# Performance work log

Measured on AMD Instinct MI355X. Metric: run time of the kernel, lower is better.

## Reference

```python
import jax, jax.numpy as jnp
import numpy as np

N = 50000       # nodes
E = 800000      # edges (before self-loops)
G = 64          # graphs in batch
F_IN = 128      # node_features
HID = 64        # hidden_channels
H1 = 8          # conv1 heads
NEG_SLOPE = 0.2
EPS = 1e-16


def _gat_layer(x, src, dst, W, att_src, att_dst, bias, heads, out_ch, concat):
    """PyG GATConv (eval mode: dropout inactive). src/dst include self-loops.
    x: [N, F_in]; W: [F_in, heads*out_ch]; att_*: [heads, out_ch]; bias: [heads*out_ch] or [out_ch]."""
    n = x.shape[0]
    h = (x @ W).reshape(n, heads, out_ch)                 # [N,H,C]
    a_s = jnp.sum(h * att_src, axis=-1)                   # [N,H]
    a_d = jnp.sum(h * att_dst, axis=-1)                   # [N,H]
    e = jax.nn.leaky_relu(a_s[src] + a_d[dst], NEG_SLOPE)  # [Etot,H]
    # segment softmax over incoming edges of each destination node
    m = jax.ops.segment_max(e, dst, num_segments=n)       # [N,H]
    e = jnp.exp(e - m[dst])
    denom = jax.ops.segment_sum(e, dst, num_segments=n)   # [N,H]
    alpha = e / (denom[dst] + EPS)                        # [Etot,H]
    msg = h[src] * alpha[:, :, None]                      # [Etot,H,C]
    out = jax.ops.segment_sum(msg, dst, num_segments=n)   # [N,H,C]
    if concat:
        out = out.reshape(n, heads * out_ch)
    else:
        out = out.mean(axis=1)
    return out + bias


def setup_inputs() -> dict:
    key = jax.random.key(0)
    ks = jax.random.split(key, 14)
    x = jax.random.normal(ks[0], (N, F_IN), dtype=jnp.float32)
    edge_index = jax.random.randint(ks[1], (2, E), 0, N, dtype=jnp.int64)
    batch_index = jnp.sort(jax.random.randint(ks[2], (N,), 0, G, dtype=jnp.int64))
    s = 0.05
    return {
        "x": x,
        "edge_index": edge_index,
        "batch_index": batch_index,
        "W1": jax.random.normal(ks[3], (F_IN, H1 * HID), dtype=jnp.float32) * s,
        "att_src1": jax.random.normal(ks[4], (H1, HID), dtype=jnp.float32) * s,
        "att_dst1": jax.random.normal(ks[5], (H1, HID), dtype=jnp.float32) * s,
        "b1": jnp.zeros((H1 * HID,), dtype=jnp.float32),
        "W2": jax.random.normal(ks[6], (H1 * HID, HID), dtype=jnp.float32) * s,
        "att_src2": jax.random.normal(ks[7], (1, HID), dtype=jnp.float32) * s,
        "att_dst2": jax.random.normal(ks[8], (1, HID), dtype=jnp.float32) * s,
        "b2": jnp.zeros((HID,), dtype=jnp.float32),
        "lin_W": jax.random.normal(ks[9], (HID, 1), dtype=jnp.float32) * s,
        "lin_b": jnp.zeros((1,), dtype=jnp.float32),
    }


def reference(x, edge_index, batch_index, W1, att_src1, att_dst1, b1,
              W2, att_src2, att_dst2, b2, lin_W, lin_b):
    n = x.shape[0]
    loops = jnp.arange(n, dtype=edge_index.dtype)
    src = jnp.concatenate([edge_index[0], loops])
    dst = jnp.concatenate([edge_index[1], loops])
    # eval mode: F.dropout is identity
    h = jax.nn.elu(_gat_layer(x, src, dst, W1, att_src1, att_dst1, b1, H1, HID, True))
    h = _gat_layer(h, src, dst, W2, att_src2, att_dst2, b2, 1, HID, False)
    # global mean pool over graphs
    sums = jax.ops.segment_sum(h, batch_index, num_segments=G)          # [G,HID]
    cnt = jax.ops.segment_sum(jnp.ones((n,), h.dtype), batch_index, num_segments=G)
    pooled = sums / jnp.maximum(cnt, 1.0)[:, None]
    return pooled @ lin_W + lin_b                                       # [G,1]
```

## Files before the change

kernel.cpp:

```cpp
#include <hip/hip_runtime.h>
#include <math.h>

#define NN 50000
#define EE 800000
#define ET 850000
#define GG 64
#define MPAD 50048
#define NCAP 64
#define NROW 50016
#define CSRI (NROW * NCAP)

typedef __attribute__((ext_vector_type(8))) short bf16x8;
typedef __attribute__((ext_vector_type(4))) float f32x4;

__device__ __forceinline__ float lrelu(float v) { return v > 0.f ? v : 0.2f * v; }

__device__ __forceinline__ unsigned short f2bf(float f) {
  unsigned u = __float_as_uint(f);
  u += 0x7FFFu + ((u >> 16) & 1u);
  return (unsigned short)(u >> 16);
}
__device__ __forceinline__ unsigned pack2(float a, float b) {
  return (unsigned)f2bf(a) | ((unsigned)f2bf(b) << 16);
}
__device__ __forceinline__ void i8acc(uint2 u, float a, float* o) {
  o[0] += a * (float)((int)(u.x << 24) >> 24);
  o[1] += a * (float)((int)(u.x << 16) >> 24);
  o[2] += a * (float)((int)(u.x <<  8) >> 24);
  o[3] += a * (float)((int)u.x >> 24);
  o[4] += a * (float)((int)(u.y << 24) >> 24);
  o[5] += a * (float)((int)(u.y << 16) >> 24);
  o[6] += a * (float)((int)(u.y <<  8) >> 24);
  o[7] += a * (float)((int)u.y >> 24);
}

#define INIT_BLOCKS 1563
#define CVT_X_BLOCKS 3128
#define CVT_W_BLOCKS 256
#define V_BLOCKS 2
#define GSEG_BLOCKS 196
__global__ __launch_bounds__(256) void prep_kernel(const float* __restrict__ x,
                                                   const float* __restrict__ W1,
                                                   const float* __restrict__ W2,
                                                   const float* __restrict__ att_s2,
                                                   const float* __restrict__ att_d2,
                                                   const float* __restrict__ linW,
                                                   const int* __restrict__ batch,
                                                   unsigned short* __restrict__ xb,
                                                   unsigned short* __restrict__ W1T,
                                                   float* __restrict__ Vs,
                                                   float* __restrict__ Vd,
                                                   float* __restrict__ Vz,
                                                   int* __restrict__ gstart,
                                                   int* __restrict__ cursor,
                                                   unsigned short* __restrict__ csr) {
  int b = blockIdx.x;
  if (b < INIT_BLOCKS) {
    int i = b * 256 + threadIdx.x;
    if (i < CSRI / 8) {
      uint4 sf = {0xC350C350u, 0xC350C350u, 0xC350C350u, 0xC350C350u};
      ((uint4*)csr)[i] = sf;
    }
    if (i < NROW) cursor[i] = 0;
  } else if (b < INIT_BLOCKS + CVT_X_BLOCKS) {
    int i8 = (b - INIT_BLOCKS) * 256 + threadIdx.x;
    if (i8 >= MPAD * 128 / 8) return;
    size_t e0 = (size_t)i8 * 8;
    int row = (int)(e0 >> 7);
    uint4 o;
    if (row < NN) {
      float4 f0 = *(const float4*)(x + e0);
      float4 f1 = *(const float4*)(x + e0 + 4);
      o.x = pack2(f0.x, f0.y); o.y = pack2(f0.z, f0.w);
      o.z = pack2(f1.x, f1.y); o.w = pack2(f1.z, f1.w);
    } else {
      o.x = o.y = o.z = o.w = 0u;
    }
    *(uint4*)(xb + e0) = o;
  } else if (b < INIT_BLOCKS + CVT_X_BLOCKS + CVT_W_BLOCKS) {
    int i = (b - INIT_BLOCKS - CVT_X_BLOCKS) * 256 + threadIdx.x;
    int k = i >> 9, n = i & 511;
    W1T[n * 128 + k] = f2bf(W1[i]);
  } else if (b < INIT_BLOCKS + CVT_X_BLOCKS + CVT_W_BLOCKS + V_BLOCKS) {
    int k = (b - INIT_BLOCKS - CVT_X_BLOCKS - CVT_W_BLOCKS) * 256 + threadIdx.x;
    float vs = 0.f, vd = 0.f, vz = 0.f;
#pragma unroll 8
    for (int c = 0; c < 64; ++c) {
      float w = W2[k * 64 + c];
      vs += w * att_s2[c];
      vd += w * att_d2[c];
      vz += w * linW[c];
    }
    Vs[k] = vs; Vd[k] = vd; Vz[k] = vz;
  } else {
    int e = (b - INIT_BLOCKS - CVT_X_BLOCKS - CVT_W_BLOCKS - V_BLOCKS) * 256 + threadIdx.x;
    if (e < NN) {
      int bb = batch[e];
      if (e == 0) {
        for (int g = 0; g <= bb; ++g) gstart[g] = 0;
      } else {
        int pb = batch[e - 1];
        for (int g = pb + 1; g <= bb; ++g) gstart[g] = e;
      }
      if (e == NN - 1) {
        for (int g = bb + 1; g <= GG; ++g) gstart[g] = NN;
      }
    }
  }
}

#define GEMM_BLOCKS 3128
#define SCAT_BLOCKS 831
#define SCAT_STRIDE (SCAT_BLOCKS * 256)
__global__ __launch_bounds__(256) void gemm1_scatter(const unsigned short* __restrict__ xb,
                                                     const unsigned short* __restrict__ W1T,
                                                     const float* __restrict__ att_s,
                                                     const float* __restrict__ att_d,
                                                     unsigned char* __restrict__ h1i,
                                                     float2* __restrict__ asc,
                                                     float* __restrict__ ad1,
                                                     const int* __restrict__ ei,
                                                     int* __restrict__ cursor,
                                                     unsigned short* __restrict__ csr) {
  __shared__ unsigned char st8[2][64 * 72];
  const int idx = blockIdx.x;
  const bool is_scat = ((idx & 3) == 3) && ((idx >> 2) < SCAT_BLOCKS);
  if (is_scat) {
    int base = (idx >> 2) * 256 + threadIdx.x;
#pragma unroll
    for (int k = 0; k < 4; ++k) {
      int e = base + k * SCAT_STRIDE;
      if (e < ET) {
        int src = (e < EE) ? ei[e] : (e - EE);
        int dst = (e < EE) ? ei[EE + e] : (e - EE);
        int pos = atomicAdd(&cursor[dst], 1);
        if (pos < NCAP) csr[(size_t)dst * NCAP + pos] = (unsigned short)src;
      }
    }
    return;
  }
  const int gi = idx - min((idx + 1) >> 2, SCAT_BLOCKS);

  const int t = threadIdx.x, w = t >> 6, l = t & 63;
  const int bm = (gi >> 2) * 64;
  const int ypair = gi & 3;
  const int m16 = l & 15, q = l >> 4;
  const int row = bm + w * 16 + m16;

  const bf16x8* Ap = (const bf16x8*)(xb + (size_t)row * 128 + q * 8);
  bf16x8 a0 = Ap[0], a1 = Ap[4], a2 = Ap[8], a3 = Ap[12];

  const int r2 = t >> 2, c16 = (t & 3) * 16;

#pragma unroll
  for (int hh = 0; hh < 2; ++hh) {
    const int h = ypair * 2 + hh;
    const bf16x8* Bp = (const bf16x8*)(W1T + (size_t)(h * 64 + m16) * 128 + q * 8);
    f32x4 acc[4] = {};
#pragma unroll
    for (int c = 0; c < 4; ++c) {
      acc[c] = __builtin_amdgcn_mfma_f32_16x16x32_bf16(a0, Bp[(size_t)c * 256 + 0],  acc[c], 0, 0, 0);
      acc[c] = __builtin_amdgcn_mfma_f32_16x16x32_bf16(a1, Bp[(size_t)c * 256 + 4],  acc[c], 0, 0, 0);
      acc[c] = __builtin_amdgcn_mfma_f32_16x16x32_bf16(a2, Bp[(size_t)c * 256 + 8],  acc[c], 0, 0, 0);
      acc[c] = __builtin_amdgcn_mfma_f32_16x16x32_bf16(a3, Bp[(size_t)c * 256 + 12], acc[c], 0, 0, 0);
    }

    float ps[4] = {0.f, 0.f, 0.f, 0.f}, pd[4] = {0.f, 0.f, 0.f, 0.f};
    float pm[4];
#pragma unroll
    for (int r = 0; r < 4; ++r)
      pm[r] = fmaxf(fmaxf(fabsf(acc[0][r]), fabsf(acc[1][r])),
                    fmaxf(fabsf(acc[2][r]), fabsf(acc[3][r])));
#pragma unroll
    for (int c = 0; c < 4; ++c) {
      float ws = att_s[h * 64 + m16 + 16 * c];
      float wd = att_d[h * 64 + m16 + 16 * c];
#pragma unroll
      for (int r = 0; r < 4; ++r) {
        ps[r] += acc[c][r] * ws;
        pd[r] += acc[c][r] * wd;
      }
    }
#pragma unroll
    for (int off = 1; off < 16; off <<= 1) {
#pragma unroll
      for (int r = 0; r < 4; ++r) {
        ps[r] += __shfl_xor(ps[r], off);
        pd[r] += __shfl_xor(pd[r], off);
        pm[r] = fmaxf(pm[r], __shfl_xor(pm[r], off));
      }
    }
    if (m16 == 0) {
#pragma unroll
      for (int r = 0; r < 4; ++r) {
        int rr = bm + w * 16 + q * 4 + r;
        float2 av;
        av.x = (rr < NN) ? ps[r] : -1e30f;
        av.y = pm[r] * (1.0f / 127.0f);
        asc[rr * 8 + h] = av;
        ad1[rr * 8 + h] = (rr < NN) ? pd[r] : 0.f;
      }
    }

    float invq[4];
#pragma unroll
    for (int r = 0; r < 4; ++r)
      invq[r] = 127.0f * __builtin_amdgcn_rcpf(fmaxf(pm[r], 1e-30f));
#pragma unroll
    for (int c = 0; c < 4; ++c)
#pragma unroll
      for (int r = 0; r < 4; ++r) {
        int qv = (int)__builtin_rintf(acc[c][r] * invq[r]);
        st8[hh][(w * 16 + q * 4 + r) * 72 + m16 + 16 * c] = (unsigned char)(qv & 0xFF);
      }
    __syncthreads();
    const unsigned* sp = (const unsigned*)(st8[hh] + r2 * 72 + c16);
    uint4 o4; o4.x = sp[0]; o4.y = sp[1]; o4.z = sp[2]; o4.w = sp[3];
    *(uint4*)(h1i + (size_t)(bm + r2) * 512 + h * 64 + c16) = o4;
  }
}

#define ISSUE8(K) do {                                                       \
    uint4 cc;                                                                \
    cc.x = __shfl(cb.x, (K)); cc.y = __shfl(cb.y, (K));                      \
    cc.z = __shfl(cb.z, (K)); cc.w = __shfl(cb.w, (K));                      \
    unsigned pr = (slot_a & 4) ? ((slot_a & 2) ? cc.w : cc.z)                \
                               : ((slot_a & 2) ? cc.y : cc.x);               \
    int my_src = (slot_a & 1) ? (int)(pr >> 16) : (int)(pr & 0xFFFFu);       \
    float2 av = asc[my_src * 8 + ha];                                        \
    asA = av.x; scA = av.y;                                                  \
    int s0 = (int)(cc.x & 0xFFFFu), s1 = (int)(cc.x >> 16);                  \
    int s2 = (int)(cc.y & 0xFFFFu), s3 = (int)(cc.y >> 16);                  \
    int s4 = (int)(cc.z & 0xFFFFu), s5 = (int)(cc.z >> 16);                  \
    int s6 = (int)(cc.w & 0xFFFFu), s7 = (int)(cc.w >> 16);                  \
    A0 = *(const uint2*)(h1i + (size_t)s0 * 512 + lane * 8);                 \
    A1 = *(const uint2*)(h1i + (size_t)s1 * 512 + lane * 8);                 \
    A2 = *(const uint2*)(h1i + (size_t)s2 * 512 + lane * 8);                 \
    A3 = *(const uint2*)(h1i + (size_t)s3 * 512 + lane * 8);                 \
    A4 = *(const uint2*)(h1i + (size_t)s4 * 512 + lane * 8);                 \
    A5 = *(const uint2*)(h1i + (size_t)s5 * 512 + lane * 8);                 \
    A6 = *(const uint2*)(h1i + (size_t)s6 * 512 + lane * 8);                 \
    A7 = *(const uint2*)(h1i + (size_t)s7 * 512 + lane * 8);                 \
  } while (0)

#define PROC8() do {                                                         \
    float myal = __expf(lrelu(asA + adv_a));                                 \
    mden += myal;                       \
    float ac = myal * scA;                                                   \
    float a0 = __shfl(ac, hb + 0), a1 = __shfl(ac, hb + 1);                  \
    float a2 = __shfl(ac, hb + 2), a3 = __shfl(ac, hb + 3);                  \
    float a4 = __shfl(ac, hb + 4), a5 = __shfl(ac, hb + 5);                  \
    float a6 = __shfl(ac, hb + 6), a7 = __shfl(ac, hb + 7);                  \
    i8acc(A0, a0, o); i8acc(A1, a1, o);                                      \
    i8acc(A2, a2, o); i8acc(A3, a3, o);                                      \
    i8acc(A4, a4, o); i8acc(A5, a5, o);                                      \
    i8acc(A6, a6, o); i8acc(A7, a7, o);                                      \
  } while (0)

__global__ __launch_bounds__(256) void agg1_kernel(const unsigned char* __restrict__ h1i,
                                                   const float2* __restrict__ asc,
                                                   const float* __restrict__ ad1,
                                                   const int* __restrict__ cnt,
                                                   const unsigned short* __restrict__ csr,
                                                   const float* __restrict__ b1,
                                                   const float* __restrict__ Vs,
                                                   const float* __restrict__ Vd,
                                                   const float* __restrict__ Vz,
                                                   float2* __restrict__ azz,
                                                   float* __restrict__ ad2) {
  int dst = blockIdx.x * 4 + (threadIdx.x >> 6);
  int lane = threadIdx.x & 63;
  if (dst >= NN) return;
  const int ha = lane >> 3;
  const int hb = ha * 8;
  const int slot_a = lane & 7;

  const int cv = min(cnt[dst], NCAP);
  const uint4 cb = *(const uint4*)(csr + (size_t)dst * NCAP + (lane & 7) * 8);
  const float adv_a = ad1[dst * 8 + ha];
  const int nb = (cv + 7) >> 3;

  float mden = 0.f;
  float o[8] = {0.f, 0.f, 0.f, 0.f, 0.f, 0.f, 0.f, 0.f};
  uint2 A0, A1, A2, A3, A4, A5, A6, A7;
  float asA, scA;

  for (int k = 0; k < nb; ++k) {
    ISSUE8(k);
    PROC8();
  }
  float den = mden;
  den += __shfl_xor(den, 1); den += __shfl_xor(den, 2); den += __shfl_xor(den, 4);
  float inv = 1.0f / (den + 1e-16f);

  const float4* bp = (const float4*)(b1 + lane * 8);
  float4 bb0 = bp[0], bb1 = bp[1];
  float bb[8] = {bb0.x, bb0.y, bb0.z, bb0.w, bb1.x, bb1.y, bb1.z, bb1.w};
  float v[8];
#pragma unroll
  for (int j = 0; j < 8; ++j) {
    float t = o[j] * inv + bb[j];
    v[j] = (t > 0.f) ? t : (__expf(t) - 1.0f);
  }

  const float4* vsp = (const float4*)(Vs + lane * 8);
  const float4* vdp = (const float4*)(Vd + lane * 8);
  const float4* vzp = (const float4*)(Vz + lane * 8);
  float4 vs0 = vsp[0], vs1 = vsp[1];
  float4 vd0 = vdp[0], vd1 = vdp[1];
  float4 vz0 = vzp[0], vz1 = vzp[1];
  float ps = v[0]*vs0.x + v[1]*vs0.y + v[2]*vs0.z + v[3]*vs0.w
           + v[4]*vs1.x + v[5]*vs1.y + v[6]*vs1.z + v[7]*vs1.w;
  float pd = v[0]*vd0.x + v[1]*vd0.y + v[2]*vd0.z + v[3]*vd0.w
           + v[4]*vd1.x + v[5]*vd1.y + v[6]*vd1.z + v[7]*vd1.w;
  float pz = v[0]*vz0.x + v[1]*vz0.y + v[2]*vz0.z + v[3]*vz0.w
           + v[4]*vz1.x + v[5]*vz1.y + v[6]*vz1.z + v[7]*vz1.w;
#pragma unroll
  for (int off = 1; off < 64; off <<= 1) {
    ps += __shfl_xor(ps, off);
    pd += __shfl_xor(pd, off);
    pz += __shfl_xor(pz, off);
  }
  if (lane == 0) {
    float2 az; az.x = ps; az.y = pz;
    azz[dst] = az;
    ad2[dst] = pd;
  }
}

__global__ __launch_bounds__(256) void agg2z_kernel(const float2* __restrict__ azz,
                                                    const float* __restrict__ ad2,
                                                    const int* __restrict__ cnt,
                                                    const unsigned short* __restrict__ csr,
                                                    float* __restrict__ s) {
  int dst = blockIdx.x * 4 + (threadIdx.x >> 6);
  int lane = threadIdx.x & 63;
  if (dst >= NN) return;
  const int si = dst * NCAP, e = si + min(cnt[dst], NCAP);
  const float adv = ad2[dst];
  float num = 0.f, den = 0.f;
  for (int i = si + lane; i < e; i += 64) {
    int src = csr[i];
    float2 az = azz[src];
    float a = __expf(lrelu(az.x + adv));
    num += a * az.y;
    den += a;
  }
#pragma unroll
  for (int off = 32; off > 0; off >>= 1) {
    num += __shfl_xor(num, off);
    den += __shfl_xor(den, off);
  }
  if (lane == 0) s[dst] = num / (den + 1e-16f);
}

__global__ __launch_bounds__(256) void poolz_kernel(const float* __restrict__ s,
                                                    const int* __restrict__ gstart,
                                                    const float* __restrict__ b2,
                                                    const float* __restrict__ linW,
                                                    const float* __restrict__ linb,
                                                    float* __restrict__ out) {
  __shared__ float red[4];
  int g = blockIdx.x;
  int t = threadIdx.x, lane = t & 63, w = t >> 6;
  int s0 = gstart[g], e0 = gstart[g + 1];
  float acc = 0.f;
  for (int i = s0 + t; i < e0; i += 256) acc += s[i];
#pragma unroll
  for (int off = 32; off > 0; off >>= 1) acc += __shfl_xor(acc, off);
  if (lane == 0) red[w] = acc;
  __syncthreads();
  if (w == 0) {
    float total = red[0] + red[1] + red[2] + red[3];
    float bz = b2[lane] * linW[lane];
#pragma unroll
    for (int off = 32; off > 0; off >>= 1) bz += __shfl_xor(bz, off);
    if (lane == 0) {
      float cnt = fmaxf((float)(e0 - s0), 1.0f);
      out[g] = total / cnt + bz + linb[0];
    }
  }
}

extern "C" void kernel_launch(void* const* d_in, const int* in_sizes, int n_in,
                              void* d_out, int out_size, void* d_ws, size_t ws_size,
                              hipStream_t stream) {
  const float* x      = (const float*)d_in[0];
  const int*   ei     = (const int*)d_in[1];
  const int*   batch  = (const int*)d_in[2];
  const float* W1     = (const float*)d_in[3];
  const float* att_s1 = (const float*)d_in[4];
  const float* att_d1 = (const float*)d_in[5];
  const float* b1     = (const float*)d_in[6];
  const float* W2     = (const float*)d_in[7];
  const float* att_s2 = (const float*)d_in[8];
  const float* att_d2 = (const float*)d_in[9];
  const float* b2     = (const float*)d_in[10];
  const float* linW   = (const float*)d_in[11];
  const float* linb   = (const float*)d_in[12];
  float* out = (float*)d_out;

  char* base = (char*)d_ws;
  unsigned short* xb  = (unsigned short*)base; base += (size_t)MPAD * 128 * 2;
  unsigned char*  h1i = (unsigned char*)base;  base += (size_t)MPAD * 512;
  unsigned short* W1T = (unsigned short*)base; base += (size_t)512 * 128 * 2;
  float* Vs   = (float*)base; base += (size_t)512 * 4;
  float* Vd   = (float*)base; base += (size_t)512 * 4;
  float* Vz   = (float*)base; base += (size_t)512 * 4;
  float2* asc = (float2*)base; base += (size_t)MPAD * 8 * 8;
  float* ad1  = (float*)base; base += (size_t)MPAD * 8 * 4;
  float2* azz = (float2*)base; base += (size_t)NROW * 8;
  float* ad2  = (float*)base; base += (size_t)NROW * 4;
  float* sv   = (float*)base; base += (size_t)NROW * 4;
  int* cursor = (int*)base;  base += (size_t)NROW * 4;
  unsigned short* csr = (unsigned short*)base; base += (size_t)CSRI * 2;
  int* gstart = (int*)base;  base += (size_t)(GG + 16) * 4;

  if (ws_size < (size_t)(base - (char*)d_ws)) return;

  prep_kernel<<<INIT_BLOCKS + CVT_X_BLOCKS + CVT_W_BLOCKS + V_BLOCKS + GSEG_BLOCKS,
                256, 0, stream>>>(x, W1, W2, att_s2, att_d2, linW, batch,
                                  xb, W1T, Vs, Vd, Vz, gstart, cursor, csr);

  gemm1_scatter<<<GEMM_BLOCKS + SCAT_BLOCKS, 256, 0, stream>>>(
      xb, W1T, att_s1, att_d1, h1i, asc, ad1, ei, cursor, csr);

  agg1_kernel<<<12500, 256, 0, stream>>>(h1i, asc, ad1, cursor, csr, b1,
                                         Vs, Vd, Vz, azz, ad2);

  agg2z_kernel<<<12500, 256, 0, stream>>>(azz, ad2, cursor, csr, sv);
  poolz_kernel<<<GG, 256, 0, stream>>>(sv, gstart, b2, linW, linb, out);
}
```

Measured before the change: 253.7 us.

## Split layer-1 aggregation by head with head-planar feature layout

Stores int8 h1 features and per-head attention scalars in head-major planes, so each aggregation block handles one head for 32 destinations, with 8 lanes per destination. The goal is a per-head working set that is small and cache-friendly (a 3.2 MB plane) when gathering neighbours. The cost is that CSR indices are re-read once per head. Per-head partial projections are written out and summed by an extra reduction kernel, which adds a launch and some intermediate traffic.

Result: slower. 289.1 us (+13.9%).

```diff
diff --git a/kernel.cpp b/kernel.cpp
--- a/kernel.cpp
+++ b/kernel.cpp
@@ -9,6 +9,7 @@
 #define NCAP 64
 #define NROW 50016
 #define CSRI (NROW * NCAP)
+#define PLANE ((size_t)MPAD * 64)
 
 typedef __attribute__((ext_vector_type(8))) short bf16x8;
 typedef __attribute__((ext_vector_type(4))) float f32x4;
@@ -197,8 +198,8 @@
         float2 av;
         av.x = (rr < NN) ? ps[r] : -1e30f;
         av.y = pm[r] * (1.0f / 127.0f);
-        asc[rr * 8 + h] = av;
-        ad1[rr * 8 + h] = (rr < NN) ? pd[r] : 0.f;
+        asc[(size_t)h * MPAD + rr] = av;
+        ad1[(size_t)h * MPAD + rr] = (rr < NN) ? pd[r] : 0.f;
       }
     }
 
@@ -216,46 +217,9 @@
     __syncthreads();
     const unsigned* sp = (const unsigned*)(st8[hh] + r2 * 72 + c16);
     uint4 o4; o4.x = sp[0]; o4.y = sp[1]; o4.z = sp[2]; o4.w = sp[3];
-    *(uint4*)(h1i + (size_t)(bm + r2) * 512 + h * 64 + c16) = o4;
-  }
-}
-
-#define ISSUE8(K) do {                                                       \
-    uint4 cc;                                                                \
-    cc.x = __shfl(cb.x, (K)); cc.y = __shfl(cb.y, (K));                      \
-    cc.z = __shfl(cb.z, (K)); cc.w = __shfl(cb.w, (K));                      \
-    unsigned pr = (slot_a & 4) ? ((slot_a & 2) ? cc.w : cc.z)                \
-                               : ((slot_a & 2) ? cc.y : cc.x);               \
-    int my_src = (slot_a & 1) ? (int)(pr >> 16) : (int)(pr & 0xFFFFu);       \
-    float2 av = asc[my_src * 8 + ha];                                        \
-    asA = av.x; scA = av.y;                                                  \
-    int s0 = (int)(cc.x & 0xFFFFu), s1 = (int)(cc.x >> 16);                  \
-    int s2 = (int)(cc.y & 0xFFFFu), s3 = (int)(cc.y >> 16);                  \
-    int s4 = (int)(cc.z & 0xFFFFu), s5 = (int)(cc.z >> 16);                  \
-    int s6 = (int)(cc.w & 0xFFFFu), s7 = (int)(cc.w >> 16);                  \
-    A0 = *(const uint2*)(h1i + (size_t)s0 * 512 + lane * 8);                 \
-    A1 = *(const uint2*)(h1i + (size_t)s1 * 512 + lane * 8);                 \
-    A2 = *(const uint2*)(h1i + (size_t)s2 * 512 + lane * 8);                 \
-    A3 = *(const uint2*)(h1i + (size_t)s3 * 512 + lane * 8);                 \
-    A4 = *(const uint2*)(h1i + (size_t)s4 * 512 + lane * 8);                 \
-    A5 = *(const uint2*)(h1i + (size_t)s5 * 512 + lane * 8);                 \
-    A6 = *(const uint2*)(h1i + (size_t)s6 * 512 + lane * 8);                 \
-    A7 = *(const uint2*)(h1i + (size_t)s7 * 512 + lane * 8);                 \
-  } while (0)
-
-#define PROC8() do {                                                         \
-    float myal = __expf(lrelu(asA + adv_a));                                 \
-    mden += myal;                       \
-    float ac = myal * scA;                                                   \
-    float a0 = __shfl(ac, hb + 0), a1 = __shfl(ac, hb + 1);                  \
-    float a2 = __shfl(ac, hb + 2), a3 = __shfl(ac, hb + 3);                  \
-    float a4 = __shfl(ac, hb + 4), a5 = __shfl(ac, hb + 5);                  \
-    float a6 = __shfl(ac, hb + 6), a7 = __shfl(ac, hb + 7);                  \
-    i8acc(A0, a0, o); i8acc(A1, a1, o);                                      \
-    i8acc(A2, a2, o); i8acc(A3, a3, o);                                      \
-    i8acc(A4, a4, o); i8acc(A5, a5, o);                                      \
-    i8acc(A6, a6, o); i8acc(A7, a7, o);                                      \
-  } while (0)
+    *(uint4*)(h1i + (size_t)h * PLANE + (size_t)(bm + r2) * 64 + c16) = o4;
+  }
+}
 
 __global__ __launch_bounds__(256) void agg1_kernel(const unsigned char* __restrict__ h1i,
                                                    const float2* __restrict__ asc,
@@ -266,35 +230,66 @@
                                                    const float* __restrict__ Vs,
                                                    const float* __restrict__ Vd,
                                                    const float* __restrict__ Vz,
-                                                   float2* __restrict__ azz,
-                                                   float* __restrict__ ad2) {
-  int dst = blockIdx.x * 4 + (threadIdx.x >> 6);
-  int lane = threadIdx.x & 63;
-  if (dst >= NN) return;
-  const int ha = lane >> 3;
-  const int hb = ha * 8;
-  const int slot_a = lane & 7;
-
-  const int cv = min(cnt[dst], NCAP);
-  const uint4 cb = *(const uint4*)(csr + (size_t)dst * NCAP + (lane & 7) * 8);
-  const float adv_a = ad1[dst * 8 + ha];
+                                                   float* __restrict__ ppS,
+                                                   float* __restrict__ ppD,
+                                                   float* __restrict__ ppZ) {
+  const int head = blockIdx.x & 7;
+  const int chunk = blockIdx.x >> 3;
+  const int lane = threadIdx.x & 63;
+  const int dsub = lane >> 3, ch8 = lane & 7;
+  const int dst = chunk * 32 + (threadIdx.x >> 6) * 8 + dsub;
+  const int dc = min(dst, NN - 1);
+
+  const unsigned char* plane = h1i + (size_t)head * PLANE + ch8 * 8;
+  const float2* ascH = asc + (size_t)head * MPAD;
+
+  const int cv = (dst < NN) ? min(cnt[dc], NCAP) : 0;
+  const float adv = ad1[(size_t)head * MPAD + dc];
+  const unsigned short* crow = csr + (size_t)dc * NCAP;
   const int nb = (cv + 7) >> 3;
 
-  float mden = 0.f;
+  float den = 0.f;
   float o[8] = {0.f, 0.f, 0.f, 0.f, 0.f, 0.f, 0.f, 0.f};
-  uint2 A0, A1, A2, A3, A4, A5, A6, A7;
-  float asA, scA;
-
-  for (int k = 0; k < nb; ++k) {
-    ISSUE8(k);
-    PROC8();
-  }
-  float den = mden;
-  den += __shfl_xor(den, 1); den += __shfl_xor(den, 2); den += __shfl_xor(den, 4);
+
+  for (int b = 0; b < nb; ++b) {
+    uint4 cc = *(const uint4*)(crow + b * 8);
+    const int lim = cv - b * 8;
+    int s0 = (0 < lim) ? (int)(cc.x & 0xFFFFu) : 0;
+    int s1 = (1 < lim) ? (int)(cc.x >> 16)     : 0;
+    int s2 = (2 < lim) ? (int)(cc.y & 0xFFFFu) : 0;
+    int s3 = (3 < lim) ? (int)(cc.y >> 16)     : 0;
+    int s4 = (4 < lim) ? (int)(cc.z & 0xFFFFu) : 0;
+    int s5 = (5 < lim) ? (int)(cc.z >> 16)     : 0;
+    int s6 = (6 < lim) ? (int)(cc.w & 0xFFFFu) : 0;
+    int s7 = (7 < lim) ? (int)(cc.w >> 16)     : 0;
+    float2 v0 = ascH[s0], v1 = ascH[s1], v2 = ascH[s2], v3 = ascH[s3];
+    float2 v4 = ascH[s4], v5 = ascH[s5], v6 = ascH[s6], v7 = ascH[s7];
+    uint2 u0 = *(const uint2*)(plane + (size_t)s0 * 64);
+    uint2 u1 = *(const uint2*)(plane + (size_t)s1 * 64);
+    uint2 u2 = *(const uint2*)(plane + (size_t)s2 * 64);
+    uint2 u3 = *(const uint2*)(plane + (size_t)s3 * 64);
+    uint2 u4 = *(const uint2*)(plane + (size_t)s4 * 64);
+    uint2 u5 = *(const uint2*)(plane + (size_t)s5 * 64);
+    uint2 u6 = *(const uint2*)(plane + (size_t)s6 * 64);
+    uint2 u7 = *(const uint2*)(plane + (size_t)s7 * 64);
+    float a0 = (0 < lim) ? __expf(lrelu(v0.x + adv)) : 0.f;
+    float a1 = (1 < lim) ? __expf(lrelu(v1.x + adv)) : 0.f;
+    float a2 = (2 < lim) ? __expf(lrelu(v2.x + adv)) : 0.f;
+    float a3 = (3 < lim) ? __expf(lrelu(v3.x + adv)) : 0.f;
+    float a4 = (4 < lim) ? __expf(lrelu(v4.x + adv)) : 0.f;
+    float a5 = (5 < lim) ? __expf(lrelu(v5.x + adv)) : 0.f;
+    float a6 = (6 < lim) ? __expf(lrelu(v6.x + adv)) : 0.f;
+    float a7 = (7 < lim) ? __expf(lrelu(v7.x + adv)) : 0.f;
+    den += ((a0 + a1) + (a2 + a3)) + ((a4 + a5) + (a6 + a7));
+    i8acc(u0, a0 * v0.y, o); i8acc(u1, a1 * v1.y, o);
+    i8acc(u2, a2 * v2.y, o); i8acc(u3, a3 * v3.y, o);
+    i8acc(u4, a4 * v4.y, o); i8acc(u5, a5 * v5.y, o);
+    i8acc(u6, a6 * v6.y, o); i8acc(u7, a7 * v7.y, o);
+  }
   float inv = 1.0f / (den + 1e-16f);
 
-  const float4* bp = (const float4*)(b1 + lane * 8);
-  float4 bb0 = bp[0], bb1 = bp[1];
+  const int cb8 = head * 64 + ch8 * 8;
+  float4 bb0 = *(const float4*)(b1 + cb8), bb1 = *(const float4*)(b1 + cb8 + 4);
   float bb[8] = {bb0.x, bb0.y, bb0.z, bb0.w, bb1.x, bb1.y, bb1.z, bb1.w};
   float v[8];
 #pragma unroll
@@ -303,29 +298,42 @@
     v[j] = (t > 0.f) ? t : (__expf(t) - 1.0f);
   }
 
-  const float4* vsp = (const float4*)(Vs + lane * 8);
-  const float4* vdp = (const float4*)(Vd + lane * 8);
-  const float4* vzp = (const float4*)(Vz + lane * 8);
-  float4 vs0 = vsp[0], vs1 = vsp[1];
-  float4 vd0 = vdp[0], vd1 = vdp[1];
-  float4 vz0 = vzp[0], vz1 = vzp[1];
+  float4 vs0 = *(const float4*)(Vs + cb8), vs1 = *(const float4*)(Vs + cb8 + 4);
+  float4 vd0 = *(const float4*)(Vd + cb8), vd1 = *(const float4*)(Vd + cb8 + 4);
+  float4 vz0 = *(const float4*)(Vz + cb8), vz1 = *(const float4*)(Vz + cb8 + 4);
   float ps = v[0]*vs0.x + v[1]*vs0.y + v[2]*vs0.z + v[3]*vs0.w
            + v[4]*vs1.x + v[5]*vs1.y + v[6]*vs1.z + v[7]*vs1.w;
   float pd = v[0]*vd0.x + v[1]*vd0.y + v[2]*vd0.z + v[3]*vd0.w
            + v[4]*vd1.x + v[5]*vd1.y + v[6]*vd1.z + v[7]*vd1.w;
   float pz = v[0]*vz0.x + v[1]*vz0.y + v[2]*vz0.z + v[3]*vz0.w
            + v[4]*vz1.x + v[5]*vz1.y + v[6]*vz1.z + v[7]*vz1.w;
-#pragma unroll
-  for (int off = 1; off < 64; off <<= 1) {
-    ps += __shfl_xor(ps, off);
-    pd += __shfl_xor(pd, off);
-    pz += __shfl_xor(pz, off);
-  }
-  if (lane == 0) {
-    float2 az; az.x = ps; az.y = pz;
-    azz[dst] = az;
-    ad2[dst] = pd;
-  }
+  ps += __shfl_xor(ps, 1); ps += __shfl_xor(ps, 2); ps += __shfl_xor(ps, 4);
+  pd += __shfl_xor(pd, 1); pd += __shfl_xor(pd, 2); pd += __shfl_xor(pd, 4);
+  pz += __shfl_xor(pz, 1); pz += __shfl_xor(pz, 2); pz += __shfl_xor(pz, 4);
+  if (ch8 == 0 && dst < NN) {
+    ppS[(size_t)head * NROW + dst] = ps;
+    ppD[(size_t)head * NROW + dst] = pd;
+    ppZ[(size_t)head * NROW + dst] = pz;
+  }
+}
+
+__global__ __launch_bounds__(256) void redu_kernel(const float* __restrict__ ppS,
+                                                   const float* __restrict__ ppD,
+                                                   const float* __restrict__ ppZ,
+                                                   float2* __restrict__ azz,
+                                                   float* __restrict__ ad2) {
+  int i = blockIdx.x * 256 + threadIdx.x;
+  if (i >= NN) return;
+  float s = 0.f, d = 0.f, z = 0.f;
+#pragma unroll
+  for (int h = 0; h < 8; ++h) {
+    s += ppS[(size_t)h * NROW + i];
+    d += ppD[(size_t)h * NROW + i];
+    z += ppZ[(size_t)h * NROW + i];
+  }
+  float2 az; az.x = s; az.y = z;
+  azz[i] = az;
+  ad2[i] = d;
 }
 
 __global__ __launch_bounds__(256) void agg2z_kernel(const float2* __restrict__ azz,
@@ -407,8 +415,11 @@
   float* Vs   = (float*)base; base += (size_t)512 * 4;
   float* Vd   = (float*)base; base += (size_t)512 * 4;
   float* Vz   = (float*)base; base += (size_t)512 * 4;
-  float2* asc = (float2*)base; base += (size_t)MPAD * 8 * 8;
-  float* ad1  = (float*)base; base += (size_t)MPAD * 8 * 4;
+  float2* asc = (float2*)base; base += (size_t)8 * MPAD * 8;
+  float* ad1  = (float*)base; base += (size_t)8 * MPAD * 4;
+  float* ppS  = (float*)base; base += (size_t)8 * NROW * 4;
+  float* ppD  = (float*)base; base += (size_t)8 * NROW * 4;
+  float* ppZ  = (float*)base; base += (size_t)8 * NROW * 4;
   float2* azz = (float2*)base; base += (size_t)NROW * 8;
   float* ad2  = (float*)base; base += (size_t)NROW * 4;
   float* sv   = (float*)base; base += (size_t)NROW * 4;
@@ -425,8 +436,9 @@
   gemm1_scatter<<<GEMM_BLOCKS + SCAT_BLOCKS, 256, 0, stream>>>(
       xb, W1T, att_s1, att_d1, h1i, asc, ad1, ei, cursor, csr);
 
-  agg1_kernel<<<12500, 256, 0, stream>>>(h1i, asc, ad1, cursor, csr, b1,
-                                         Vs, Vd, Vz, azz, ad2);
+  agg1_kernel<<<8 * 1563, 256, 0, stream>>>(h1i, asc, ad1, cursor, csr, b1,
+                                            Vs, Vd, Vz, ppS, ppD, ppZ);
+  redu_kernel<<<196, 256, 0, stream>>>(ppS, ppD, ppZ, azz, ad2);
 
   agg2z_kernel<<<12500, 256, 0, stream>>>(azz, ad2, cursor, csr, sv);
   poolz_kernel<<<GG, 256, 0, stream>>>(sv, gstart, b2, linW, linb, out);
```
